# Kernel optimization log

Measured on AMD Instinct MI355X. Metric: run time of the kernel, lower is better.

The kernel has to match this reference:

```python
import jax, jax.numpy as jnp
import numpy as np

EPS_NORM = 1e-12  # F.normalize eps
EPS_BN = 1e-5     # BatchNorm eps


def setup_inputs() -> dict:
    key = jax.random.key(0)
    ks = jax.random.split(key, 8)
    B, N, P, d = 64, 4, 128, 256  # batch, subgraphs, patches/subgraph, feature_dim
    h = 256                        # hidden2[-1]
    C = 2                          # num_class
    totP = N * P                   # 512 == num_patches
    feat = totP * h                # readout size = 131072

    def w(k, shape, s=0.02):
        return jax.random.normal(k, shape, dtype=jnp.float32) * s

    return {
        "x": jax.random.normal(ks[0], (B, totP, d), dtype=jnp.float32),
        "edge_prior_mask": jax.random.uniform(ks[1], (P, P), dtype=jnp.float32),
        # stage1 GCN layers (Linear stored as [in, out])
        "W1": w(ks[2], (d, h)), "b1": jnp.zeros((h,), jnp.float32),
        "g1": jnp.ones((h,), jnp.float32), "be1": jnp.zeros((h,), jnp.float32),
        "W2": w(ks[3], (h, h)), "b2": jnp.zeros((h,), jnp.float32),
        "g2": jnp.ones((h,), jnp.float32), "be2": jnp.zeros((h,), jnp.float32),
        # mlp_causal
        "Wm1": w(ks[4], (feat, 128), 0.005), "bm1": jnp.zeros((128,), jnp.float32),
        "gm1": jnp.ones((128,), jnp.float32), "bem1": jnp.zeros((128,), jnp.float32),
        "Wm2": w(ks[5], (128, 64)), "bm2": jnp.zeros((64,), jnp.float32),
        "gm2": jnp.ones((64,), jnp.float32), "bem2": jnp.zeros((64,), jnp.float32),
        "Wm3": w(ks[6], (64, C)), "bm3": jnp.zeros((C,), jnp.float32),
    }


def reference(x, edge_prior_mask, W1, b1, g1, be1, W2, b2, g2, be2,
              Wm1, bm1, gm1, bem1, Wm2, bm2, gm2, bem2, Wm3, bm3):
    B, totP, d = x.shape
    P = edge_prior_mask.shape[0]
    N = totP // P

    # ---- dynamic edges: per-subgraph cosine similarity * prior mask ----
    xb = x.reshape(B, N, P, d)
    nrm = jnp.linalg.norm(xb, axis=-1, keepdims=True)
    xn = xb / jnp.maximum(nrm, EPS_NORM)
    sim = (jnp.einsum('bnpd,bnqd->bnpq', xn, xn) + 1.0) * 0.5  # [B,N,P,P]
    blocks = sim * edge_prior_mask[None, None]

    # block-diagonal assembly [B, totP, totP]
    edges = jnp.zeros((B, totP, totP), dtype=x.dtype)
    for i in range(N):
        edges = edges.at[:, i * P:(i + 1) * P, i * P:(i + 1) * P].set(blocks[:, i])
    eye = jnp.eye(totP, dtype=x.dtype)
    edges = edges * (1.0 - eye)  # zero the diagonal

    # ---- symmetric degree normalization with self loops ----
    A = edges + eye
    deg = A.sum(-1)  # [B, totP]
    dinv = jnp.where(deg > 0, 1.0 / jnp.sqrt(jnp.maximum(deg, EPS_NORM)), 0.0)
    An = dinv[:, :, None] * A * dinv[:, None, :]

    # ---- two GCN layers: bmm(An, X @ W + b) -> BN (over batch+nodes) -> relu ----
    def bn_relu(hh, g, b):
        m = hh.mean(axis=(0, 1), keepdims=True)
        v = hh.var(axis=(0, 1), keepdims=True)
        return jax.nn.relu(g * (hh - m) / jnp.sqrt(v + EPS_BN) + b)

    h1 = bn_relu(jnp.einsum('bpq,bqh->bph', An, x @ W1 + b1), g1, be1)
    h2 = bn_relu(jnp.einsum('bpq,bqh->bph', An, h1 @ W2 + b2), g2, be2)

    # ---- readout + MLP head (dropout = identity in eval) ----
    graph = h2.reshape(B, -1)

    def bn1d(z, g, b):
        m = z.mean(0, keepdims=True)
        v = z.var(0, keepdims=True)
        return g * (z - m) / jnp.sqrt(v + EPS_BN) + b

    z = jax.nn.relu(bn1d(graph @ Wm1 + bm1, gm1, bem1))
    z = jax.nn.relu(bn1d(z @ Wm2 + bm2, gm2, bem2))
    return z @ Wm3 + bm3
```

## Files before the change

### kernel.cpp

```cpp
#include <hip/hip_runtime.h>
#include <cstdint>
#include <cstddef>

#define P_    128
#define H_    256
#define FEAT_ 131072

__global__ __launch_bounds__(256) void k_xn(
    const float* __restrict__ x, float* __restrict__ xn) {
  const int t = threadIdx.x;
  const int lane = t & 63;
  const int row = blockIdx.x * 4 + (t >> 6);
  const float* xr = x + (size_t)row * 256;
  const float4 v = *(const float4*)(xr + lane * 4);
  float ss = v.x * v.x + v.y * v.y + v.z * v.z + v.w * v.w;
  #pragma unroll
  for (int s = 32; s; s >>= 1) ss += __shfl_xor(ss, s, 64);
  const float inv = 1.0f / fmaxf(sqrtf(ss), 1e-12f);
  *(float4*)(xn + (size_t)row * 256 + lane * 4) =
      make_float4(v.x * inv, v.y * inv, v.z * inv, v.w * inv);
}

__global__ __launch_bounds__(256) void k_simfused(
    const float* __restrict__ xn, const float* __restrict__ mask,
    float* __restrict__ An) {
  __shared__ float Xs[16][128];
  __shared__ float red[128][17];
  __shared__ float dinv_s[128];
  const int blk = blockIdx.x;
  const int t = threadIdx.x;
  const int tp = t >> 4, tq = t & 15;
  const float* Xb = xn + (size_t)blk * (128 * 256);

  float v[8][8];
  #pragma unroll
  for (int i = 0; i < 8; ++i)
    #pragma unroll
    for (int j = 0; j < 8; ++j) v[i][j] = 0.f;

  for (int kc = 0; kc < 16; ++kc) {
    __syncthreads();
    #pragma unroll
    for (int l = 0; l < 2; ++l) {
      const int f = t + 256 * l;
      const int row = f >> 2, k4 = (f & 3) * 4;
      const float4 x4 = *(const float4*)(Xb + (size_t)row * 256 + kc * 16 + k4);
      Xs[k4 + 0][row] = x4.x;
      Xs[k4 + 1][row] = x4.y;
      Xs[k4 + 2][row] = x4.z;
      Xs[k4 + 3][row] = x4.w;
    }
    __syncthreads();
    #pragma unroll
    for (int k = 0; k < 16; ++k) {
      const float4 a0 = *(const float4*)&Xs[k][tp * 8];
      const float4 a1 = *(const float4*)&Xs[k][tp * 8 + 4];
      const float4 b0 = *(const float4*)&Xs[k][tq * 8];
      const float4 b1 = *(const float4*)&Xs[k][tq * 8 + 4];
      const float a[8] = {a0.x, a0.y, a0.z, a0.w, a1.x, a1.y, a1.z, a1.w};
      const float b[8] = {b0.x, b0.y, b0.z, b0.w, b1.x, b1.y, b1.z, b1.w};
      #pragma unroll
      for (int i = 0; i < 8; ++i)
        #pragma unroll
        for (int j = 0; j < 8; ++j) v[i][j] += a[i] * b[j];
    }
  }

  #pragma unroll
  for (int i = 0; i < 8; ++i) {
    const int r = tp * 8 + i;
    const float4 m0 = *(const float4*)(mask + r * 128 + tq * 8);
    const float4 m1 = *(const float4*)(mask + r * 128 + tq * 8 + 4);
    const float mm[8] = {m0.x, m0.y, m0.z, m0.w, m1.x, m1.y, m1.z, m1.w};
    float s = 0.f;
    #pragma unroll
    for (int j = 0; j < 8; ++j) {
      const int c = tq * 8 + j;
      const float vv = (r == c) ? 0.0f : (v[i][j] + 1.0f) * 0.5f * mm[j];
      v[i][j] = vv;
      s += vv;
    }
    red[r][tq] = s;
  }
  __syncthreads();
  if (t < 128) {
    float sm = 0.f;
    #pragma unroll
    for (int u = 0; u < 16; ++u) sm += red[t][u];
    const float deg = 1.0f + sm;
    dinv_s[t] = (deg > 0.0f) ? rsqrtf(fmaxf(deg, 1e-12f)) : 0.0f;
  }
  __syncthreads();

  float dq[8];
  #pragma unroll
  for (int j = 0; j < 8; ++j) dq[j] = dinv_s[tq * 8 + j];
  float* Ab = An + (size_t)blk * 16384;
  #pragma unroll
  for (int i = 0; i < 8; ++i) {
    const int r = tp * 8 + i;
    const float dp = dinv_s[r];
    float o[8];
    #pragma unroll
    for (int j = 0; j < 8; ++j) {
      const int c = tq * 8 + j;
      o[j] = (r == c) ? dp * dq[j] : v[i][j] * dp * dq[j];
    }
    *(float4*)(Ab + (size_t)r * 128 + tq * 8)     = make_float4(o[0], o[1], o[2], o[3]);
    *(float4*)(Ab + (size_t)r * 128 + tq * 8 + 4) = make_float4(o[4], o[5], o[6], o[7]);
  }
}

__global__ __launch_bounds__(256) void k_gemm_t(
    const float* __restrict__ A, const float* __restrict__ W,
    const float* __restrict__ bias, float* __restrict__ out) {
  __shared__ float As[16][128];
  __shared__ float Ws[16][128];
  const int rb = blockIdx.x, cb = blockIdx.y;
  const int t = threadIdx.x, tp = t >> 4, tq = t & 15;
  const int m0 = rb * 128, c0 = cb * 128;

  float acc[8][8];
  #pragma unroll
  for (int j = 0; j < 8; ++j) {
    const float bj = bias[c0 + tq * 8 + j];
    #pragma unroll
    for (int i = 0; i < 8; ++i) acc[i][j] = bj;
  }

  for (int kc = 0; kc < 16; ++kc) {
    __syncthreads();
    #pragma unroll
    for (int l = 0; l < 2; ++l) {
      const int f = t + 256 * l;
      const int row = f >> 2, k4 = (f & 3) * 4;
      const float4 a4 = *(const float4*)(A + (size_t)(m0 + row) * 256 + kc * 16 + k4);
      As[k4 + 0][row] = a4.x;
      As[k4 + 1][row] = a4.y;
      As[k4 + 2][row] = a4.z;
      As[k4 + 3][row] = a4.w;
    }
    #pragma unroll
    for (int l = 0; l < 2; ++l) {
      const int f = t + 256 * l;
      const int k = f >> 5, c4 = (f & 31) * 4;
      const float4 w4 = *(const float4*)(W + (size_t)(kc * 16 + k) * 256 + c0 + c4);
      *(float4*)&Ws[k][c4] = w4;
    }
    __syncthreads();
    #pragma unroll
    for (int k = 0; k < 16; ++k) {
      const float4 a0 = *(const float4*)&As[k][tp * 8];
      const float4 a1 = *(const float4*)&As[k][tp * 8 + 4];
      const float4 w0 = *(const float4*)&Ws[k][tq * 8];
      const float4 w1 = *(const float4*)&Ws[k][tq * 8 + 4];
      const float a[8] = {a0.x, a0.y, a0.z, a0.w, a1.x, a1.y, a1.z, a1.w};
      const float w[8] = {w0.x, w0.y, w0.z, w0.w, w1.x, w1.y, w1.z, w1.w};
      #pragma unroll
      for (int i = 0; i < 8; ++i)
        #pragma unroll
        for (int j = 0; j < 8; ++j) acc[i][j] += a[i] * w[j];
    }
  }

  #pragma unroll
  for (int i = 0; i < 8; ++i) {
    float* orow = out + (size_t)(m0 + tp * 8 + i) * 256 + c0 + tq * 8;
    *(float4*)(orow)     = make_float4(acc[i][0], acc[i][1], acc[i][2], acc[i][3]);
    *(float4*)(orow + 4) = make_float4(acc[i][4], acc[i][5], acc[i][6], acc[i][7]);
  }
}

__global__ __launch_bounds__(256) void k_gemmbn_t(
    const float* __restrict__ A, const float* __restrict__ scsh,
    const float* __restrict__ W, const float* __restrict__ bias,
    float* __restrict__ out) {
  __shared__ float As[16][128];
  __shared__ float Ws[16][128];
  const int rb = blockIdx.x, cb = blockIdx.y;
  const int t = threadIdx.x, tp = t >> 4, tq = t & 15;
  const int m0 = rb * 128, c0 = cb * 128;

  float acc[8][8];
  #pragma unroll
  for (int j = 0; j < 8; ++j) {
    const float bj = bias[c0 + tq * 8 + j];
    #pragma unroll
    for (int i = 0; i < 8; ++i) acc[i][j] = bj;
  }

  for (int kc = 0; kc < 16; ++kc) {
    __syncthreads();
    #pragma unroll
    for (int l = 0; l < 2; ++l) {
      const int f = t + 256 * l;
      const int row = f >> 2, k4 = (f & 3) * 4;
      const int col = kc * 16 + k4;
      const float4 a4 = *(const float4*)(A + (size_t)(m0 + row) * 256 + col);
      const float4 sc = *(const float4*)(scsh + col);
      const float4 sh = *(const float4*)(scsh + 256 + col);
      As[k4 + 0][row] = fmaxf(a4.x * sc.x + sh.x, 0.0f);
      As[k4 + 1][row] = fmaxf(a4.y * sc.y + sh.y, 0.0f);
      As[k4 + 2][row] = fmaxf(a4.z * sc.z + sh.z, 0.0f);
      As[k4 + 3][row] = fmaxf(a4.w * sc.w + sh.w, 0.0f);
    }
    #pragma unroll
    for (int l = 0; l < 2; ++l) {
      const int f = t + 256 * l;
      const int k = f >> 5, c4 = (f & 31) * 4;
      const float4 w4 = *(const float4*)(W + (size_t)(kc * 16 + k) * 256 + c0 + c4);
      *(float4*)&Ws[k][c4] = w4;
    }
    __syncthreads();
    #pragma unroll
    for (int k = 0; k < 16; ++k) {
      const float4 a0 = *(const float4*)&As[k][tp * 8];
      const float4 a1 = *(const float4*)&As[k][tp * 8 + 4];
      const float4 w0 = *(const float4*)&Ws[k][tq * 8];
      const float4 w1 = *(const float4*)&Ws[k][tq * 8 + 4];
      const float a[8] = {a0.x, a0.y, a0.z, a0.w, a1.x, a1.y, a1.z, a1.w};
      const float w[8] = {w0.x, w0.y, w0.z, w0.w, w1.x, w1.y, w1.z, w1.w};
      #pragma unroll
      for (int i = 0; i < 8; ++i)
        #pragma unroll
        for (int j = 0; j < 8; ++j) acc[i][j] += a[i] * w[j];
    }
  }

  #pragma unroll
  for (int i = 0; i < 8; ++i) {
    float* orow = out + (size_t)(m0 + tp * 8 + i) * 256 + c0 + tq * 8;
    *(float4*)(orow)     = make_float4(acc[i][0], acc[i][1], acc[i][2], acc[i][3]);
    *(float4*)(orow + 4) = make_float4(acc[i][4], acc[i][5], acc[i][6], acc[i][7]);
  }
}

__global__ __launch_bounds__(256) void k_bmmst(
    const float* __restrict__ An, const float* __restrict__ XW,
    float* __restrict__ out, float* __restrict__ part) {
  __shared__ float As[16][128];
  __shared__ float Ws[16][128];
  __shared__ float rs[16][128];
  __shared__ float rq[16][128];
  const int blk = blockIdx.x, cb = blockIdx.y;
  const int t = threadIdx.x, tp = t >> 4, tq = t & 15;
  const float* Ab = An + (size_t)blk * 16384;
  const float* Xb = XW + (size_t)blk * (128 * 256);

  float acc[8][8];
  #pragma unroll
  for (int i = 0; i < 8; ++i)
    #pragma unroll
    for (int j = 0; j < 8; ++j) acc[i][j] = 0.f;

  for (int kc = 0; kc < 8; ++kc) {
    __syncthreads();
    #pragma unroll
    for (int l = 0; l < 2; ++l) {
      const int f = t + 256 * l;
      const int row = f >> 2, k4 = (f & 3) * 4;
      const float4 a4 = *(const float4*)(Ab + (size_t)row * 128 + kc * 16 + k4);
      As[k4 + 0][row] = a4.x;
      As[k4 + 1][row] = a4.y;
      As[k4 + 2][row] = a4.z;
      As[k4 + 3][row] = a4.w;
    }
    #pragma unroll
    for (int l = 0; l < 2; ++l) {
      const int f = t + 256 * l;
      const int k = f >> 5, c4 = (f & 31) * 4;
      const float4 w4 = *(const float4*)(Xb + (size_t)(kc * 16 + k) * 256 + cb * 128 + c4);
      *(float4*)&Ws[k][c4] = w4;
    }
    __syncthreads();
    #pragma unroll
    for (int k = 0; k < 16; ++k) {
      const float4 a0 = *(const float4*)&As[k][tp * 8];
      const float4 a1 = *(const float4*)&As[k][tp * 8 + 4];
      const float4 w0 = *(const float4*)&Ws[k][tq * 8];
      const float4 w1 = *(const float4*)&Ws[k][tq * 8 + 4];
      const float a[8] = {a0.x, a0.y, a0.z, a0.w, a1.x, a1.y, a1.z, a1.w};
      const float w[8] = {w0.x, w0.y, w0.z, w0.w, w1.x, w1.y, w1.z, w1.w};
      #pragma unroll
      for (int i = 0; i < 8; ++i)
        #pragma unroll
        for (int j = 0; j < 8; ++j) acc[i][j] += a[i] * w[j];
    }
  }

  #pragma unroll
  for (int j = 0; j < 8; ++j) {
    float cs = 0.f, cq = 0.f;
    #pragma unroll
    for (int i = 0; i < 8; ++i) { cs += acc[i][j]; cq += acc[i][j] * acc[i][j]; }
    rs[tp][tq * 8 + j] = cs;
    rq[tp][tq * 8 + j] = cq;
  }
  __syncthreads();
  if (t < 128) {
    float s = 0.f, q = 0.f;
    #pragma unroll
    for (int u = 0; u < 16; ++u) { s += rs[u][t]; q += rq[u][t]; }
    const int base = (blk * 2 + cb) * 256;
    part[base + t]       = s;
    part[base + 128 + t] = q;
  }

  #pragma unroll
  for (int i = 0; i < 8; ++i) {
    float* orow = out + (size_t)(blk * 128 + tp * 8 + i) * 256 + cb * 128 + tq * 8;
    *(float4*)(orow)     = make_float4(acc[i][0], acc[i][1], acc[i][2], acc[i][3]);
    *(float4*)(orow + 4) = make_float4(acc[i][4], acc[i][5], acc[i][6], acc[i][7]);
  }
}

__global__ __launch_bounds__(256) void k_bnscsh(
    const float* __restrict__ part, const float* __restrict__ g,
    const float* __restrict__ be, float* __restrict__ scsh) {
  const int c = threadIdx.x;
  const int cb = c >> 7, lc = c & 127;
  float s = 0.f, q = 0.f;
  for (int blk = 0; blk < 256; ++blk) {
    const float* pb = part + (size_t)(blk * 2 + cb) * 256;
    s += pb[lc];
    q += pb[128 + lc];
  }
  const float m = s * (1.0f / 32768.0f);
  const float var = q * (1.0f / 32768.0f) - m * m;
  const float sc = g[c] * rsqrtf(var + 1e-5f);
  scsh[c] = sc;
  scsh[256 + c] = be[c] - m * sc;
}

__global__ __launch_bounds__(256) void k_headgemm_v3(
    const float* __restrict__ pre2, const float* __restrict__ scsh,
    const float* __restrict__ Wm1, float* __restrict__ part) {
  __shared__ float graphS[64][128];
  const int t = threadIdx.x;
  const int bid = blockIdx.x;
  const int k0 = bid * 128;
  const int cbase = k0 & 255;

  #pragma unroll
  for (int l = 0; l < 8; ++l) {
    const int f = t + 256 * l;
    const int row = f >> 5, c4 = (f & 31) * 4;
    const float4 p = *(const float4*)(pre2 + (size_t)row * FEAT_ + k0 + c4);
    const float4 sc = *(const float4*)(scsh + cbase + c4);
    const float4 sh = *(const float4*)(scsh + 256 + cbase + c4);
    graphS[row][c4 + 0] = fmaxf(p.x * sc.x + sh.x, 0.0f);
    graphS[row][c4 + 1] = fmaxf(p.y * sc.y + sh.y, 0.0f);
    graphS[row][c4 + 2] = fmaxf(p.z * sc.z + sh.z, 0.0f);
    graphS[row][c4 + 3] = fmaxf(p.w * sc.w + sh.w, 0.0f);
  }
  __syncthreads();

  const int hg = t & 31;
  const int bg = t >> 5;
  float acc[8][4];
  #pragma unroll
  for (int i = 0; i < 8; ++i)
    #pragma unroll
    for (int j = 0; j < 4; ++j) acc[i][j] = 0.f;

  #pragma unroll 2
  for (int kk = 0; kk < 128; kk += 4) {
    const int k = k0 + kk;
    const float4 w0 = *(const float4*)(Wm1 + (size_t)(k + 0) * 128 + hg * 4);
    const float4 w1 = *(const float4*)(Wm1 + (size_t)(k + 1) * 128 + hg * 4);
    const float4 w2 = *(const float4*)(Wm1 + (size_t)(k + 2) * 128 + hg * 4);
    const float4 w3 = *(const float4*)(Wm1 + (size_t)(k + 3) * 128 + hg * 4);
    #pragma unroll
    for (int i = 0; i < 8; ++i) {
      const float4 a = *(const float4*)&graphS[bg * 8 + i][kk];
      acc[i][0] += a.x * w0.x; acc[i][1] += a.x * w0.y;
      acc[i][2] += a.x * w0.z; acc[i][3] += a.x * w0.w;
      acc[i][0] += a.y * w1.x; acc[i][1] += a.y * w1.y;
      acc[i][2] += a.y * w1.z; acc[i][3] += a.y * w1.w;
      acc[i][0] += a.z * w2.x; acc[i][1] += a.z * w2.y;
      acc[i][2] += a.z * w2.z; acc[i][3] += a.z * w2.w;
      acc[i][0] += a.w * w3.x; acc[i][1] += a.w * w3.y;
      acc[i][2] += a.w * w3.z; acc[i][3] += a.w * w3.w;
    }
  }

  float* pb = part + (size_t)bid * 8192;
  #pragma unroll
  for (int i = 0; i < 8; ++i)
    *(float4*)(pb + (bg * 8 + i) * 128 + hg * 4) =
        make_float4(acc[i][0], acc[i][1], acc[i][2], acc[i][3]);
}

__global__ __launch_bounds__(256) void k_headredA(
    const float* __restrict__ part, float* __restrict__ part2) {
  const int o = blockIdx.x * 256 + threadIdx.x;
  const int jg = blockIdx.y;
  const float* base = part + (size_t)jg * 128 * 8192;
  float s = 0.f;
  for (int j = 0; j < 128; ++j) s += base[(size_t)j * 8192 + o];
  part2[(size_t)jg * 8192 + o] = s;
}

__global__ __launch_bounds__(256) void k_headredB(
    const float* __restrict__ part2, float* __restrict__ z1) {
  const int o = blockIdx.x * 256 + threadIdx.x;
  float s = 0.f;
  #pragma unroll
  for (int jg = 0; jg < 8; ++jg) s += part2[(size_t)jg * 8192 + o];
  z1[o] = s;
}

template <int J>
__global__ __launch_bounds__(64) void k_headbn(
    const float* __restrict__ z, const float* __restrict__ g,
    const float* __restrict__ be, float* __restrict__ zr) {
  __shared__ float rs[64], rs2[64];
  const int j = blockIdx.x, b = threadIdx.x;
  const float v = z[b * J + j];
  rs[b] = v; rs2[b] = v * v; __syncthreads();
  for (int s = 32; s; s >>= 1) {
    if (b < s) { rs[b] += rs[b + s]; rs2[b] += rs2[b + s]; }
    __syncthreads();
  }
  const float m = rs[0] * (1.0f / 64.0f);
  const float var = rs2[0] * (1.0f / 64.0f) - m * m;
  const float sc = g[j] * rsqrtf(var + 1e-5f);
  const float sh = be[j] - m * sc;
  zr[b * J + j] = fmaxf(v * sc + sh, 0.0f);
}

__global__ __launch_bounds__(64) void k_headmm2(
    const float* __restrict__ zr1, const float* __restrict__ Wm2,
    float* __restrict__ z2) {
  const int b = blockIdx.x, j = threadIdx.x;
  float acc = 0.f;
  for (int k = 0; k < 128; ++k) acc += zr1[b * 128 + k] * Wm2[k * 64 + j];
  z2[b * 64 + j] = acc;
}

__global__ __launch_bounds__(128) void k_headout(
    const float* __restrict__ zr2, const float* __restrict__ Wm3,
    const float* __restrict__ bm3, float* __restrict__ out) {
  const int t = threadIdx.x;
  const int b = t >> 1, c = t & 1;
  float s = bm3[c];
  for (int k = 0; k < 64; ++k) s += zr2[b * 64 + k] * Wm3[k * 2 + c];
  out[t] = s;
}

extern "C" void kernel_launch(void* const* d_in, const int* in_sizes, int n_in,
                              void* d_out, int out_size, void* d_ws, size_t ws_size,
                              hipStream_t stream) {
  (void)in_sizes; (void)n_in; (void)out_size; (void)ws_size;
  const float* x    = (const float*)d_in[0];
  const float* mask = (const float*)d_in[1];
  const float* W1   = (const float*)d_in[2];
  const float* b1   = (const float*)d_in[3];
  const float* g1   = (const float*)d_in[4];
  const float* be1  = (const float*)d_in[5];
  const float* W2   = (const float*)d_in[6];
  const float* b2   = (const float*)d_in[7];
  const float* g2   = (const float*)d_in[8];
  const float* be2  = (const float*)d_in[9];
  const float* Wm1  = (const float*)d_in[10];
  const float* gm1  = (const float*)d_in[12];
  const float* bem1 = (const float*)d_in[13];
  const float* Wm2  = (const float*)d_in[14];
  const float* gm2  = (const float*)d_in[16];
  const float* bem2 = (const float*)d_in[17];
  const float* Wm3  = (const float*)d_in[18];
  const float* bm3  = (const float*)d_in[19];

  float* ws   = (float*)d_ws;
  float* T1   = ws;
  float* An   = T1 + 8388608;
  float* T2   = An + 4194304;
  float* T3   = T2 + 8388608;
  float* z1   = T3 + 8388608;
  float* dinv = z1 + 8192;
  float* st1  = dinv + 32768;
  float* st2  = st1 + 512;
  float* zr1  = st2 + 512;
  float* z2   = zr1 + 8192;
  float* zr2  = z2 + 4096;

  float* scsh1 = dinv;
  float* scsh2 = dinv + 512;

  k_xn<<<8192, 256, 0, stream>>>(x, T1);
  k_simfused<<<256, 256, 0, stream>>>(T1, mask, An);

  k_gemm_t<<<dim3(256, 2), 256, 0, stream>>>(x, W1, b1, T2);
  k_bmmst<<<dim3(256, 2), 256, 0, stream>>>(An, T2, T3, T1);
  k_bnscsh<<<1, 256, 0, stream>>>(T1, g1, be1, scsh1);

  k_gemmbn_t<<<dim3(256, 2), 256, 0, stream>>>(T3, scsh1, W2, b2, T2);
  k_bmmst<<<dim3(256, 2), 256, 0, stream>>>(An, T2, T3, T1);
  k_bnscsh<<<1, 256, 0, stream>>>(T1, g2, be2, scsh2);

  k_headgemm_v3<<<1024, 256, 0, stream>>>(T3, scsh2, Wm1, T2);
  k_headredA<<<dim3(32, 8), 256, 0, stream>>>(T2, An);
  k_headredB<<<32, 256, 0, stream>>>(An, z1);
  k_headbn<128><<<128, 64, 0, stream>>>(z1, gm1, bem1, zr1);
  k_headmm2<<<64, 64, 0, stream>>>(zr1, Wm2, z2);
  k_headbn<64><<<64, 64, 0, stream>>>(z2, gm2, bem2, zr2);
  k_headout<<<1, 128, 0, stream>>>(zr2, Wm3, bm3, (float*)d_out);
}
```

Measured before the change: 458.1 us.

## Halve GEMM row tiles for more blocks and parallelize BN stat reduction

The GCN GEMM and batched-matmul kernels now use 64x128 output tiles with 4x8 accumulators per thread, doubling the grid and cutting register pressure. Column mapping is split into two 64-wide halves, and BN partial sums are written per row-half. The BN scale/shift kernel now uses one block per channel with a shared-memory tree reduction instead of a single block looping serially. The trade-off is lower reuse per tile, more global loads of the weight tiles, and twice the partial-stat data.

```diff
diff --git a/kernel.cpp b/kernel.cpp
--- a/kernel.cpp
+++ b/kernel.cpp
@@ -114,26 +114,25 @@
 __global__ __launch_bounds__(256) void k_gemm_t(
     const float* __restrict__ A, const float* __restrict__ W,
     const float* __restrict__ bias, float* __restrict__ out) {
-  __shared__ float As[16][128];
+  __shared__ float As[16][64];
   __shared__ float Ws[16][128];
   const int rb = blockIdx.x, cb = blockIdx.y;
   const int t = threadIdx.x, tp = t >> 4, tq = t & 15;
-  const int m0 = rb * 128, c0 = cb * 128;
-
-  float acc[8][8];
+  const int m0 = rb * 64, c0 = cb * 128;
+
+  float acc[4][8];
   #pragma unroll
   for (int j = 0; j < 8; ++j) {
-    const float bj = bias[c0 + tq * 8 + j];
-    #pragma unroll
-    for (int i = 0; i < 8; ++i) acc[i][j] = bj;
+    const int col = c0 + ((j < 4) ? (tq * 4 + j) : (64 + tq * 4 + j - 4));
+    const float bj = bias[col];
+    #pragma unroll
+    for (int i = 0; i < 4; ++i) acc[i][j] = bj;
   }
 
   for (int kc = 0; kc < 16; ++kc) {
     __syncthreads();
-    #pragma unroll
-    for (int l = 0; l < 2; ++l) {
-      const int f = t + 256 * l;
-      const int row = f >> 2, k4 = (f & 3) * 4;
+    {
+      const int row = t >> 2, k4 = (t & 3) * 4;
       const float4 a4 = *(const float4*)(A + (size_t)(m0 + row) * 256 + kc * 16 + k4);
       As[k4 + 0][row] = a4.x;
       As[k4 + 1][row] = a4.y;
@@ -144,30 +143,29 @@
     for (int l = 0; l < 2; ++l) {
       const int f = t + 256 * l;
       const int k = f >> 5, c4 = (f & 31) * 4;
-      const float4 w4 = *(const float4*)(W + (size_t)(kc * 16 + k) * 256 + c0 + c4);
-      *(float4*)&Ws[k][c4] = w4;
+      *(float4*)&Ws[k][c4] =
+          *(const float4*)(W + (size_t)(kc * 16 + k) * 256 + c0 + c4);
     }
     __syncthreads();
     #pragma unroll
     for (int k = 0; k < 16; ++k) {
-      const float4 a0 = *(const float4*)&As[k][tp * 8];
-      const float4 a1 = *(const float4*)&As[k][tp * 8 + 4];
-      const float4 w0 = *(const float4*)&Ws[k][tq * 8];
-      const float4 w1 = *(const float4*)&Ws[k][tq * 8 + 4];
-      const float a[8] = {a0.x, a0.y, a0.z, a0.w, a1.x, a1.y, a1.z, a1.w};
+      const float4 av = *(const float4*)&As[k][tp * 4];
+      const float4 w0 = *(const float4*)&Ws[k][tq * 4];
+      const float4 w1 = *(const float4*)&Ws[k][64 + tq * 4];
+      const float a[4] = {av.x, av.y, av.z, av.w};
       const float w[8] = {w0.x, w0.y, w0.z, w0.w, w1.x, w1.y, w1.z, w1.w};
       #pragma unroll
-      for (int i = 0; i < 8; ++i)
+      for (int i = 0; i < 4; ++i)
         #pragma unroll
         for (int j = 0; j < 8; ++j) acc[i][j] += a[i] * w[j];
     }
   }
 
   #pragma unroll
-  for (int i = 0; i < 8; ++i) {
-    float* orow = out + (size_t)(m0 + tp * 8 + i) * 256 + c0 + tq * 8;
-    *(float4*)(orow)     = make_float4(acc[i][0], acc[i][1], acc[i][2], acc[i][3]);
-    *(float4*)(orow + 4) = make_float4(acc[i][4], acc[i][5], acc[i][6], acc[i][7]);
+  for (int i = 0; i < 4; ++i) {
+    float* orow = out + (size_t)(m0 + tp * 4 + i) * 256 + c0;
+    *(float4*)(orow + tq * 4)      = make_float4(acc[i][0], acc[i][1], acc[i][2], acc[i][3]);
+    *(float4*)(orow + 64 + tq * 4) = make_float4(acc[i][4], acc[i][5], acc[i][6], acc[i][7]);
   }
 }
 
@@ -175,26 +173,25 @@
     const float* __restrict__ A, const float* __restrict__ scsh,
     const float* __restrict__ W, const float* __restrict__ bias,
     float* __restrict__ out) {
-  __shared__ float As[16][128];
+  __shared__ float As[16][64];
   __shared__ float Ws[16][128];
   const int rb = blockIdx.x, cb = blockIdx.y;
   const int t = threadIdx.x, tp = t >> 4, tq = t & 15;
-  const int m0 = rb * 128, c0 = cb * 128;
-
-  float acc[8][8];
+  const int m0 = rb * 64, c0 = cb * 128;
+
+  float acc[4][8];
   #pragma unroll
   for (int j = 0; j < 8; ++j) {
-    const float bj = bias[c0 + tq * 8 + j];
-    #pragma unroll
-    for (int i = 0; i < 8; ++i) acc[i][j] = bj;
+    const int col = c0 + ((j < 4) ? (tq * 4 + j) : (64 + tq * 4 + j - 4));
+    const float bj = bias[col];
+    #pragma unroll
+    for (int i = 0; i < 4; ++i) acc[i][j] = bj;
   }
 
   for (int kc = 0; kc < 16; ++kc) {
     __syncthreads();
-    #pragma unroll
-    for (int l = 0; l < 2; ++l) {
-      const int f = t + 256 * l;
-      const int row = f >> 2, k4 = (f & 3) * 4;
+    {
+      const int row = t >> 2, k4 = (t & 3) * 4;
       const int col = kc * 16 + k4;
       const float4 a4 = *(const float4*)(A + (size_t)(m0 + row) * 256 + col);
       const float4 sc = *(const float4*)(scsh + col);
@@ -208,57 +205,56 @@
     for (int l = 0; l < 2; ++l) {
       const int f = t + 256 * l;
       const int k = f >> 5, c4 = (f & 31) * 4;
-      const float4 w4 = *(const float4*)(W + (size_t)(kc * 16 + k) * 256 + c0 + c4);
-      *(float4*)&Ws[k][c4] = w4;
+      *(float4*)&Ws[k][c4] =
+          *(const float4*)(W + (size_t)(kc * 16 + k) * 256 + c0 + c4);
     }
     __syncthreads();
     #pragma unroll
     for (int k = 0; k < 16; ++k) {
-      const float4 a0 = *(const float4*)&As[k][tp * 8];
-      const float4 a1 = *(const float4*)&As[k][tp * 8 + 4];
-      const float4 w0 = *(const float4*)&Ws[k][tq * 8];
-      const float4 w1 = *(const float4*)&Ws[k][tq * 8 + 4];
-      const float a[8] = {a0.x, a0.y, a0.z, a0.w, a1.x, a1.y, a1.z, a1.w};
+      const float4 av = *(const float4*)&As[k][tp * 4];
+      const float4 w0 = *(const float4*)&Ws[k][tq * 4];
+      const float4 w1 = *(const float4*)&Ws[k][64 + tq * 4];
+      const float a[4] = {av.x, av.y, av.z, av.w};
       const float w[8] = {w0.x, w0.y, w0.z, w0.w, w1.x, w1.y, w1.z, w1.w};
       #pragma unroll
-      for (int i = 0; i < 8; ++i)
+      for (int i = 0; i < 4; ++i)
         #pragma unroll
         for (int j = 0; j < 8; ++j) acc[i][j] += a[i] * w[j];
     }
   }
 
   #pragma unroll
-  for (int i = 0; i < 8; ++i) {
-    float* orow = out + (size_t)(m0 + tp * 8 + i) * 256 + c0 + tq * 8;
-    *(float4*)(orow)     = make_float4(acc[i][0], acc[i][1], acc[i][2], acc[i][3]);
-    *(float4*)(orow + 4) = make_float4(acc[i][4], acc[i][5], acc[i][6], acc[i][7]);
+  for (int i = 0; i < 4; ++i) {
+    float* orow = out + (size_t)(m0 + tp * 4 + i) * 256 + c0;
+    *(float4*)(orow + tq * 4)      = make_float4(acc[i][0], acc[i][1], acc[i][2], acc[i][3]);
+    *(float4*)(orow + 64 + tq * 4) = make_float4(acc[i][4], acc[i][5], acc[i][6], acc[i][7]);
   }
 }
 
 __global__ __launch_bounds__(256) void k_bmmst(
     const float* __restrict__ An, const float* __restrict__ XW,
     float* __restrict__ out, float* __restrict__ part) {
-  __shared__ float As[16][128];
+  __shared__ float As[16][64];
   __shared__ float Ws[16][128];
   __shared__ float rs[16][128];
   __shared__ float rq[16][128];
-  const int blk = blockIdx.x, cb = blockIdx.y;
+  const int blk = blockIdx.x;
+  const int y = blockIdx.y;
+  const int rh = y >> 1, cb = y & 1;
   const int t = threadIdx.x, tp = t >> 4, tq = t & 15;
-  const float* Ab = An + (size_t)blk * 16384;
+  const float* Ab = An + (size_t)blk * 16384 + (size_t)rh * 64 * 128;
   const float* Xb = XW + (size_t)blk * (128 * 256);
 
-  float acc[8][8];
-  #pragma unroll
-  for (int i = 0; i < 8; ++i)
+  float acc[4][8];
+  #pragma unroll
+  for (int i = 0; i < 4; ++i)
     #pragma unroll
     for (int j = 0; j < 8; ++j) acc[i][j] = 0.f;
 
   for (int kc = 0; kc < 8; ++kc) {
     __syncthreads();
-    #pragma unroll
-    for (int l = 0; l < 2; ++l) {
-      const int f = t + 256 * l;
-      const int row = f >> 2, k4 = (f & 3) * 4;
+    {
+      const int row = t >> 2, k4 = (t & 3) * 4;
       const float4 a4 = *(const float4*)(Ab + (size_t)row * 128 + kc * 16 + k4);
       As[k4 + 0][row] = a4.x;
       As[k4 + 1][row] = a4.y;
@@ -269,20 +265,19 @@
     for (int l = 0; l < 2; ++l) {
       const int f = t + 256 * l;
       const int k = f >> 5, c4 = (f & 31) * 4;
-      const float4 w4 = *(const float4*)(Xb + (size_t)(kc * 16 + k) * 256 + cb * 128 + c4);
-      *(float4*)&Ws[k][c4] = w4;
+      *(float4*)&Ws[k][c4] =
+          *(const float4*)(Xb + (size_t)(kc * 16 + k) * 256 + cb * 128 + c4);
     }
     __syncthreads();
     #pragma unroll
     for (int k = 0; k < 16; ++k) {
-      const float4 a0 = *(const float4*)&As[k][tp * 8];
-      const float4 a1 = *(const float4*)&As[k][tp * 8 + 4];
-      const float4 w0 = *(const float4*)&Ws[k][tq * 8];
-      const float4 w1 = *(const float4*)&Ws[k][tq * 8 + 4];
-      const float a[8] = {a0.x, a0.y, a0.z, a0.w, a1.x, a1.y, a1.z, a1.w};
+      const float4 av = *(const float4*)&As[k][tp * 4];
+      const float4 w0 = *(const float4*)&Ws[k][tq * 4];
+      const float4 w1 = *(const float4*)&Ws[k][64 + tq * 4];
+      const float a[4] = {av.x, av.y, av.z, av.w};
       const float w[8] = {w0.x, w0.y, w0.z, w0.w, w1.x, w1.y, w1.z, w1.w};
       #pragma unroll
-      for (int i = 0; i < 8; ++i)
+      for (int i = 0; i < 4; ++i)
         #pragma unroll
         for (int j = 0; j < 8; ++j) acc[i][j] += a[i] * w[j];
     }
@@ -292,44 +287,52 @@
   for (int j = 0; j < 8; ++j) {
     float cs = 0.f, cq = 0.f;
     #pragma unroll
-    for (int i = 0; i < 8; ++i) { cs += acc[i][j]; cq += acc[i][j] * acc[i][j]; }
-    rs[tp][tq * 8 + j] = cs;
-    rq[tp][tq * 8 + j] = cq;
+    for (int i = 0; i < 4; ++i) { cs += acc[i][j]; cq += acc[i][j] * acc[i][j]; }
+    const int col = (j < 4) ? (tq * 4 + j) : (64 + tq * 4 + j - 4);
+    rs[tp][col] = cs;
+    rq[tp][col] = cq;
   }
   __syncthreads();
   if (t < 128) {
     float s = 0.f, q = 0.f;
     #pragma unroll
     for (int u = 0; u < 16; ++u) { s += rs[u][t]; q += rq[u][t]; }
-    const int base = (blk * 2 + cb) * 256;
+    const int base = (blk * 4 + y) * 256;
     part[base + t]       = s;
     part[base + 128 + t] = q;
   }
 
   #pragma unroll
-  for (int i = 0; i < 8; ++i) {
-    float* orow = out + (size_t)(blk * 128 + tp * 8 + i) * 256 + cb * 128 + tq * 8;
-    *(float4*)(orow)     = make_float4(acc[i][0], acc[i][1], acc[i][2], acc[i][3]);
-    *(float4*)(orow + 4) = make_float4(acc[i][4], acc[i][5], acc[i][6], acc[i][7]);
+  for (int i = 0; i < 4; ++i) {
+    float* orow = out + (size_t)(blk * 128 + rh * 64 + tp * 4 + i) * 256 + cb * 128;
+    *(float4*)(orow + tq * 4)      = make_float4(acc[i][0], acc[i][1], acc[i][2], acc[i][3]);
+    *(float4*)(orow + 64 + tq * 4) = make_float4(acc[i][4], acc[i][5], acc[i][6], acc[i][7]);
   }
 }
 
 __global__ __launch_bounds__(256) void k_bnscsh(
     const float* __restrict__ part, const float* __restrict__ g,
     const float* __restrict__ be, float* __restrict__ scsh) {
-  const int c = threadIdx.x;
+  __shared__ float ss[256], qq[256];
+  const int c = blockIdx.x;
   const int cb = c >> 7, lc = c & 127;
-  float s = 0.f, q = 0.f;
-  for (int blk = 0; blk < 256; ++blk) {
-    const float* pb = part + (size_t)(blk * 2 + cb) * 256;
-    s += pb[lc];
-    q += pb[128 + lc];
-  }
-  const float m = s * (1.0f / 32768.0f);
-  const float var = q * (1.0f / 32768.0f) - m * m;
-  const float sc = g[c] * rsqrtf(var + 1e-5f);
-  scsh[c] = sc;
-  scsh[256 + c] = be[c] - m * sc;
+  const int u = threadIdx.x;
+  const float* p0 = part + (size_t)(u * 4 + cb) * 256;
+  const float* p1 = part + (size_t)(u * 4 + 2 + cb) * 256;
+  ss[u] = p0[lc] + p1[lc];
+  qq[u] = p0[128 + lc] + p1[128 + lc];
+  __syncthreads();
+  for (int st = 128; st; st >>= 1) {
+    if (u < st) { ss[u] += ss[u + st]; qq[u] += qq[u + st]; }
+    __syncthreads();
+  }
+  if (u == 0) {
+    const float m = ss[0] * (1.0f / 32768.0f);
+    const float var = qq[0] * (1.0f / 32768.0f) - m * m;
+    const float sc = g[c] * rsqrtf(var + 1e-5f);
+    scsh[c] = sc;
+    scsh[256 + c] = be[c] - m * sc;
+  }
 }
 
 __global__ __launch_bounds__(256) void k_headgemm_v3(
@@ -490,13 +493,13 @@
   k_xn<<<8192, 256, 0, stream>>>(x, T1);
   k_simfused<<<256, 256, 0, stream>>>(T1, mask, An);
 
-  k_gemm_t<<<dim3(256, 2), 256, 0, stream>>>(x, W1, b1, T2);
-  k_bmmst<<<dim3(256, 2), 256, 0, stream>>>(An, T2, T3, T1);
-  k_bnscsh<<<1, 256, 0, stream>>>(T1, g1, be1, scsh1);
-
-  k_gemmbn_t<<<dim3(256, 2), 256, 0, stream>>>(T3, scsh1, W2, b2, T2);
-  k_bmmst<<<dim3(256, 2), 256, 0, stream>>>(An, T2, T3, T1);
-  k_bnscsh<<<1, 256, 0, stream>>>(T1, g2, be2, scsh2);
+  k_gemm_t<<<dim3(512, 2), 256, 0, stream>>>(x, W1, b1, T2);
+  k_bmmst<<<dim3(256, 4), 256, 0, stream>>>(An, T2, T3, T1);
+  k_bnscsh<<<256, 256, 0, stream>>>(T1, g1, be1, scsh1);
+
+  k_gemmbn_t<<<dim3(512, 2), 256, 0, stream>>>(T3, scsh1, W2, b2, T2);
+  k_bmmst<<<dim3(256, 4), 256, 0, stream>>>(An, T2, T3, T1);
+  k_bnscsh<<<256, 256, 0, stream>>>(T1, g2, be2, scsh2);
 
   k_headgemm_v3<<<1024, 256, 0, stream>>>(T3, scsh2, Wm1, T2);
   k_headredA<<<dim3(32, 8), 256, 0, stream>>>(T2, An);
```

Result: faster. 439.2 us (-4.1%).
